# Kernel tuning notes

Measured on AMD Instinct MI355X. Metric: run time of the kernel, lower is better.

## Reference

```python
import jax, jax.numpy as jnp
import numpy as np

G = 8  # num_group
EPS = 1e-6


def setup_inputs() -> dict:
    key = jax.random.key(0)
    k1, k2 = jax.random.split(key)
    B, K, CG = 4, 8192, 1024
    kpts = jax.random.normal(k1, (B, K, 2), dtype=jnp.float32)
    desc = jax.random.uniform(k2, (B, K, CG), dtype=jnp.float32)
    return {"kpts": kpts, "desc": desc}


def reference(kpts, desc):
    """DescGroupPoolandNorm.desc_pool_and_norm_infer with pool='shift',
    candidate='top1', norm='l2'. Returns (kpts_update, desc_update)."""
    B, K, CG = desc.shape
    C = CG // G
    d = desc.reshape(B, K, C, G)
    # top-1 shift per keypoint from the first channel group: [B, K]
    s = jnp.argmax(d[:, :, 0, :], axis=-1)
    # torch.roll(d, shifts=-s, dims=-1): out[..., j] = d[..., (j + s) % G]
    idx = (jnp.arange(G)[None, None, None, :] + s[:, :, None, None]) % G  # [B,K,1,G]
    rolled = jnp.take_along_axis(d, jnp.broadcast_to(idx, (B, K, C, G)), axis=-1)
    desc_update = rolled.reshape(B, K, CG)  # topk=1 -> [B, 1*K, CG]
    # L2Norm with eps
    norm = jnp.linalg.norm(desc_update, axis=-1) + EPS
    desc_update = desc_update / norm[..., None]
    kpts_update = kpts  # kpts.repeat(1, topk=1, 1)
    return kpts_update, desc_update
```

## Files before the change

kernel.cpp:

```cpp
#include <hip/hip_runtime.h>
#include <math.h>


#define ROWLEN 1024

typedef float f32x4 __attribute__((ext_vector_type(4)));

__device__ __forceinline__ void nt_store4(float4 v, float4* p) {
    f32x4 w = {v.x, v.y, v.z, v.w};
    __builtin_nontemporal_store(w, (f32x4*)p);
}

template<int S>
__device__ __forceinline__ void roll_pair(const float4 a0, const float4 a1,
                                          const float inv,
                                          float4& o0, float4& o1) {
    const float f[8] = {a0.x, a0.y, a0.z, a0.w, a1.x, a1.y, a1.z, a1.w};
    o0.x = f[(S + 0) & 7] * inv;
    o0.y = f[(S + 1) & 7] * inv;
    o0.z = f[(S + 2) & 7] * inv;
    o0.w = f[(S + 3) & 7] * inv;
    o1.x = f[(S + 4) & 7] * inv;
    o1.y = f[(S + 5) & 7] * inv;
    o1.z = f[(S + 6) & 7] * inv;
    o1.w = f[(S + 7) & 7] * inv;
}

#define ROLL_CASE(S)                                                 \
    case S:                                                          \
        roll_pair<S>(a0, a1, inv, o0, o1);                           \
        roll_pair<S>(b0, b1, inv, o2, o3);                           \
        break;

__global__ __launch_bounds__(256) void REDFM_15676630630653_kernel(
    const float* __restrict__ desc, float* __restrict__ out,
    const float* __restrict__ kpts, float* __restrict__ kpts_out,
    int rows, int descBlocks) {
    if (blockIdx.x >= descBlocks) {
        const int i = (blockIdx.x - descBlocks) * 256 + threadIdx.x;
        const float4 v = ((const float4*)kpts)[i];
        nt_store4(v, ((float4*)kpts_out) + i);
        return;
    }

    const int gtid = blockIdx.x * 256 + threadIdx.x;
    const int r = gtid >> 6;
    const int lane = threadIdx.x & 63;

    const float4* __restrict__ row = (const float4*)(desc + (size_t)r * ROWLEN);
    float4* __restrict__ orow = (float4*)(out + (size_t)r * ROWLEN);

    const float4 a0 = row[2 * lane];
    const float4 a1 = row[2 * lane + 1];
    const float4 b0 = row[2 * lane + 128];
    const float4 b1 = row[2 * lane + 129];

    float ss = a0.x * a0.x + a0.y * a0.y + a0.z * a0.z + a0.w * a0.w
             + a1.x * a1.x + a1.y * a1.y + a1.z * a1.z + a1.w * a1.w
             + b0.x * b0.x + b0.y * b0.y + b0.z * b0.z + b0.w * b0.w
             + b1.x * b1.x + b1.y * b1.y + b1.z * b1.z + b1.w * b1.w;
#pragma unroll
    for (int off = 1; off < 64; off <<= 1) ss += __shfl_xor(ss, off);
    const float inv = 1.0f / (sqrtf(ss) + 1e-6f);

    const float vals[8] = {a0.x, a0.y, a0.z, a0.w, a1.x, a1.y, a1.z, a1.w};
    int bi = 0;
    float bv = vals[0];
#pragma unroll
    for (int m = 1; m < 8; m++) {
        if (vals[m] > bv) { bv = vals[m]; bi = m; }
    }
    const int s = __builtin_amdgcn_readfirstlane(bi);

    float4 o0, o1, o2, o3;
    switch (s) {
        ROLL_CASE(0)
        ROLL_CASE(1)
        ROLL_CASE(2)
        ROLL_CASE(3)
        ROLL_CASE(4)
        ROLL_CASE(5)
        ROLL_CASE(6)
        ROLL_CASE(7)
        default: o0 = o1 = o2 = o3 = make_float4(0.f, 0.f, 0.f, 0.f); break;
    }

    nt_store4(o0, orow + 2 * lane);
    nt_store4(o1, orow + 2 * lane + 1);
    nt_store4(o2, orow + 2 * lane + 128);
    nt_store4(o3, orow + 2 * lane + 129);
}

extern "C" void kernel_launch(void* const* d_in, const int* in_sizes, int n_in,
                              void* d_out, int out_size, void* d_ws, size_t ws_size,
                              hipStream_t stream) {
    const float* kpts = (const float*)d_in[0];
    const float* desc = (const float*)d_in[1];
    float* out = (float*)d_out;

    const int kpts_elems = in_sizes[0];
    const int desc_elems = in_sizes[1];
    const int rows = desc_elems / ROWLEN;

    float* desc_out = out + kpts_elems;
    const int descBlocks = (rows * 64 + 255) / 256;
    const int kptsBlocks = (kpts_elems / 4 + 255) / 256;
    REDFM_15676630630653_kernel<<<descBlocks + kptsBlocks, 256, 0, stream>>>(
        desc, desc_out, kpts, out, rows, descBlocks);
}
```

Before: 52.36 us.

## Process four rows per wavefront with register prefetch and plain stores

Each wavefront now handles four consecutive rows, loading the next row into registers while the current row is normalized and rolled. This cuts the grid size by four and is meant to overlap load latency with compute and stores. It also swaps nontemporal stores for ordinary stores, which changes cache behaviour for the large streaming output. The trade-off is fewer waves in flight and higher register pressure.

```diff
diff --git a/kernel.cpp b/kernel.cpp
--- a/kernel.cpp
+++ b/kernel.cpp
@@ -3,13 +3,7 @@
 
 
 #define ROWLEN 1024
-
-typedef float f32x4 __attribute__((ext_vector_type(4)));
-
-__device__ __forceinline__ void nt_store4(float4 v, float4* p) {
-    f32x4 w = {v.x, v.y, v.z, v.w};
-    __builtin_nontemporal_store(w, (f32x4*)p);
-}
+#define RPW 4
 
 template<int S>
 __device__ __forceinline__ void roll_pair(const float4 a0, const float4 a1,
@@ -32,29 +26,10 @@
         roll_pair<S>(b0, b1, inv, o2, o3);                           \
         break;
 
-__global__ __launch_bounds__(256) void REDFM_15676630630653_kernel(
-    const float* __restrict__ desc, float* __restrict__ out,
-    const float* __restrict__ kpts, float* __restrict__ kpts_out,
-    int rows, int descBlocks) {
-    if (blockIdx.x >= descBlocks) {
-        const int i = (blockIdx.x - descBlocks) * 256 + threadIdx.x;
-        const float4 v = ((const float4*)kpts)[i];
-        nt_store4(v, ((float4*)kpts_out) + i);
-        return;
-    }
-
-    const int gtid = blockIdx.x * 256 + threadIdx.x;
-    const int r = gtid >> 6;
-    const int lane = threadIdx.x & 63;
-
-    const float4* __restrict__ row = (const float4*)(desc + (size_t)r * ROWLEN);
-    float4* __restrict__ orow = (float4*)(out + (size_t)r * ROWLEN);
-
-    const float4 a0 = row[2 * lane];
-    const float4 a1 = row[2 * lane + 1];
-    const float4 b0 = row[2 * lane + 128];
-    const float4 b1 = row[2 * lane + 129];
-
+__device__ __forceinline__ void process_row(const float4 a0, const float4 a1,
+                                            const float4 b0, const float4 b1,
+                                            float4* __restrict__ orow,
+                                            const int lane) {
     float ss = a0.x * a0.x + a0.y * a0.y + a0.z * a0.z + a0.w * a0.w
              + a1.x * a1.x + a1.y * a1.y + a1.z * a1.z + a1.w * a1.w
              + b0.x * b0.x + b0.y * b0.y + b0.z * b0.z + b0.w * b0.w
@@ -85,10 +60,48 @@
         default: o0 = o1 = o2 = o3 = make_float4(0.f, 0.f, 0.f, 0.f); break;
     }
 
-    nt_store4(o0, orow + 2 * lane);
-    nt_store4(o1, orow + 2 * lane + 1);
-    nt_store4(o2, orow + 2 * lane + 128);
-    nt_store4(o3, orow + 2 * lane + 129);
+    orow[2 * lane] = o0;
+    orow[2 * lane + 1] = o1;
+    orow[2 * lane + 128] = o2;
+    orow[2 * lane + 129] = o3;
+}
+
+__global__ __launch_bounds__(256) void REDFM_15676630630653_kernel(
+    const float* __restrict__ desc, float* __restrict__ out,
+    const float* __restrict__ kpts, float* __restrict__ kpts_out,
+    int rows, int descBlocks) {
+    if (blockIdx.x >= descBlocks) {
+        const int i = (blockIdx.x - descBlocks) * 256 + threadIdx.x;
+        ((float4*)kpts_out)[i] = ((const float4*)kpts)[i];
+        return;
+    }
+
+    const int wid = (blockIdx.x * 256 + threadIdx.x) >> 6;
+    const int lane = threadIdx.x & 63;
+    const int r0 = wid * RPW;
+    if (r0 >= rows) return;
+
+    const float4* __restrict__ rowp = (const float4*)(desc + (size_t)r0 * ROWLEN);
+
+    float4 c0 = rowp[2 * lane];
+    float4 c1 = rowp[2 * lane + 1];
+    float4 c2 = rowp[2 * lane + 128];
+    float4 c3 = rowp[2 * lane + 129];
+
+#pragma unroll
+    for (int i = 0; i < RPW; i++) {
+        float4 n0, n1, n2, n3;
+        if (i + 1 < RPW) {
+            const float4* np = rowp + (size_t)(i + 1) * (ROWLEN / 4);
+            n0 = np[2 * lane];
+            n1 = np[2 * lane + 1];
+            n2 = np[2 * lane + 128];
+            n3 = np[2 * lane + 129];
+        }
+        process_row(c0, c1, c2, c3,
+                    (float4*)(out + (size_t)(r0 + i) * ROWLEN), lane);
+        if (i + 1 < RPW) { c0 = n0; c1 = n1; c2 = n2; c3 = n3; }
+    }
 }
 
 extern "C" void kernel_launch(void* const* d_in, const int* in_sizes, int n_in,
@@ -103,7 +116,8 @@
     const int rows = desc_elems / ROWLEN;
 
     float* desc_out = out + kpts_elems;
-    const int descBlocks = (rows * 64 + 255) / 256;
+    const int rowsPerBlock = 4 * RPW;
+    const int descBlocks = (rows + rowsPerBlock - 1) / rowsPerBlock;
     const int kptsBlocks = (kpts_elems / 4 + 255) / 256;
     REDFM_15676630630653_kernel<<<descBlocks + kptsBlocks, 256, 0, stream>>>(
         desc, desc_out, kpts, out, rows, descBlocks);
```

Result: no change. 52.02 us (-0.6%).
